# Kernel tuning notes

Measured on AMD Instinct MI355X. Metric: run time of the kernel, lower is better.

Reference implementation:

```python
import jax, jax.numpy as jnp
import numpy as np

V0, V1, V2 = 8000, 4000, 4096   # diag / proc / med vocab sizes
E = 512                          # emb_dim
T, L = 64, 48                    # visits, codes per visit
FAI = 0.05                       # history-selection threshold
EPS = 1e-5                       # LayerNorm eps (torch default)

def _normalize(adj):
    # GCN.normalize: row-normalize (adj + I)
    adj = adj + np.eye(adj.shape[0], dtype=np.float64)
    rowsum = adj.sum(1)
    r_inv = np.where(rowsum > 0, 1.0 / rowsum, 0.0)
    return (r_inv[:, None] * adj).astype(np.float32)

def setup_inputs() -> dict:
    key = jax.random.key(0)
    ks = iter(jax.random.split(key, 48))
    p = lambda *s: jax.random.normal(next(ks), s, jnp.float32) * 0.02
    rng = np.random.default_rng(0)
    def rand_adj():
        a = rng.random((V2, V2)) < 0.01
        a = (a | a.T).astype(np.float64)
        np.fill_diagonal(a, 0.0)
        return a
    ehr = rand_adj(); ddi = rand_adj()
    return dict(
        diag_codes=jax.random.randint(next(ks), (T, L), 0, V0),
        proc_codes=jax.random.randint(next(ks), (T, L), 0, V1),
        emb0=p(V0, E), emb1=p(V1, E), emb2=p(V2, E),
        gru1_Wih=p(3 * E, E), gru1_Whh=p(3 * E, E), gru1_bih=p(3 * E), gru1_bhh=p(3 * E),
        gru2_Wih=p(3 * E, E), gru2_Whh=p(3 * E, E), gru2_bih=p(3 * E), gru2_bhh=p(3 * E),
        query_W=p(E, 2 * E), query_b=p(E),
        poly_h1_W=p(32, 2 * E), poly_h1_b=p(32), poly_gate_W=p(1, 32), poly_gate_b=p(1),
        cls_W=p(V2, 2 * E), cls_b=p(V2),
        ln_gamma=jnp.ones((E,), jnp.float32), ln_beta=jnp.zeros((E,), jnp.float32),
        ehr_W1=p(V2, E), ehr_b1=p(E), ehr_W2=p(E, E), ehr_b2=p(E),
        ddi_W1=p(V2, E), ddi_b1=p(E), ddi_W2=p(E, E), ddi_b2=p(E),
        inter1=p(1),
        ehr_adj_norm=jnp.asarray(_normalize(ehr)),
        ddi_adj_norm=jnp.asarray(_normalize(ddi)),
        ddi_adj=jnp.asarray(ddi.astype(np.float32)),
    )

def _gru_last(x_seq, mask, Wih, Whh, bih, bhh):
    # torch nn.GRU cell, batch=1; masked-out steps carry h unchanged, which
    # equals running the GRU over only the selected subsequence. Only the
    # final hidden state is needed (original uses output[-1]).
    def step(h, inp):
        x, m = inp
        gi = x @ Wih.T + bih          # [3E]
        gh = h @ Whh.T + bhh
        ir, iz, inn = jnp.split(gi, 3)
        hr, hz, hn = jnp.split(gh, 3)
        r = jax.nn.sigmoid(ir + hr)
        z = jax.nn.sigmoid(iz + hz)
        n = jnp.tanh(inn + r * hn)
        h_new = (1.0 - z) * n + z * h
        return jnp.where(m, h_new, h), None
    h0 = jnp.zeros((Wih.shape[1],), x_seq.dtype)
    h_final, _ = jax.lax.scan(step, h0, (x_seq, mask))
    return h_final

def reference(diag_codes, proc_codes, emb0, emb1, emb2,
              gru1_Wih, gru1_Whh, gru1_bih, gru1_bhh,
              gru2_Wih, gru2_Whh, gru2_bih, gru2_bhh,
              query_W, query_b, poly_h1_W, poly_h1_b, poly_gate_W, poly_gate_b,
              cls_W, cls_b, ln_gamma, ln_beta,
              ehr_W1, ehr_b1, ehr_W2, ehr_b2, ddi_W1, ddi_b1, ddi_W2, ddi_b2,
              inter1, ehr_adj_norm, ddi_adj_norm, ddi_adj):
    i1 = emb0[diag_codes].sum(1)            # [T,E] per-visit sum pooling
    i2 = emb1[proc_codes].sum(1)            # [T,E]
    rep = jnp.concatenate([i1, i2], -1)     # [T,2E] patient representation
    # Aggregation gate for history selection
    hidden = jax.nn.relu(rep @ poly_h1_W.T + poly_h1_b)
    gate = jax.nn.sigmoid(hidden @ poly_gate_W.T + poly_gate_b)[:, 0]  # [T]
    s = jnp.abs(gate[-1] - gate[:-1])
    mask = jnp.concatenate([s <= FAI, jnp.ones((1,), bool)])  # last visit always kept
    h1 = _gru_last(i1, mask, gru1_Wih, gru1_Whh, gru1_bih, gru1_bhh)
    h2 = _gru_last(i2, mask, gru2_Wih, gru2_Whh, gru2_bih, gru2_bhh)
    q_in = jnp.concatenate([h1, h2])                      # [2E]
    query = (jax.nn.relu(q_in) @ query_W.T + query_b)[None, :]  # [1,E]
    def gcn(W1, b1, W2, b2, adj):
        h = jax.nn.relu(adj @ W1 + b1)    # x = I so x@W1 = W1 (dropout eval)
        return adj @ (h @ W2) + b2
    safe = gcn(ehr_W1, ehr_b1, ehr_W2, ehr_b2, ehr_adj_norm) \
         - inter1 * gcn(ddi_W1, ddi_b1, ddi_W2, ddi_b2, ddi_adj_norm)
    drug = safe + emb2                                    # [V2,E]
    kw = jax.nn.softmax(query @ drug.T, -1)               # [1,V2]
    med = kw @ drug                                       # [1,E]
    mu = query.mean(-1, keepdims=True)
    var = ((query - mu) ** 2).mean(-1, keepdims=True)
    ln = (query - mu) / jnp.sqrt(var + EPS) * ln_gamma + ln_beta
    final = jnp.concatenate([ln, med], -1)                # [1,2E]
    result = jax.nn.relu(final) @ cls_W.T + cls_b         # [1,V2]
    neg = jax.nn.sigmoid(result)
    batch_neg = 0.0005 * ((neg.T * neg) * ddi_adj).sum()
    return result, batch_neg
```

## Files before the change

### kernel.cpp

```cpp
#include <hip/hip_runtime.h>
#include <cstdint>
#include <cstddef>

typedef unsigned short u16;
typedef unsigned int   u32;

typedef __bf16 bf16x8 __attribute__((ext_vector_type(8)));
typedef float  f32x4  __attribute__((ext_vector_type(4)));

__device__ __forceinline__ float uAsF(u32 u){ union{u32 u; float f;} c; c.u=u; return c.f; }
__device__ __forceinline__ float b2f(u16 v){ return uAsF(((u32)v)<<16); }
__device__ __forceinline__ u16 f2b(float f){
  union{float f; u32 u;} c; c.f=f; u32 x=c.u;
  u32 r = (x + 0x7fffu + ((x>>16)&1u)) >> 16;
  return (u16)r;
}
__device__ __forceinline__ void unpack8(uint4 p, float* f){
  f[0]=uAsF(p.x<<16); f[1]=uAsF(p.x&0xffff0000u);
  f[2]=uAsF(p.y<<16); f[3]=uAsF(p.y&0xffff0000u);
  f[4]=uAsF(p.z<<16); f[5]=uAsF(p.z&0xffff0000u);
  f[6]=uAsF(p.w<<16); f[7]=uAsF(p.w&0xffff0000u);
}
__device__ __forceinline__ float sigm(float x){ return 1.f/(1.f+__expf(-x)); }

// ... 15 lines not shown
}
__device__ __forceinline__ void ld4(const void* p, size_t i, int f32, float* f){
  if (f32){
    float4 a = *(const float4*)((const float*)p + i);
    f[0]=a.x; f[1]=a.y; f[2]=a.z; f[3]=a.w;
  } else {
    uint2 pk = *(const uint2*)((const u16*)p + i);
    f[0]=uAsF(pk.x<<16); f[1]=uAsF(pk.x&0xffff0000u);
    f[2]=uAsF(pk.y<<16); f[3]=uAsF(pk.y&0xffff0000u);
  }
}
__device__ __forceinline__ uint4 ld8p(const void* p, size_t i, int f32){
  if (f32){
    const float4* q = (const float4*)((const float*)p + i);
    float4 a = q[0], b = q[1];
    uint4 r;
    r.x = (u32)f2b(a.x) | ((u32)f2b(a.y)<<16);
    r.y = (u32)f2b(a.z) | ((u32)f2b(a.w)<<16);
    r.z = (u32)f2b(b.x) | ((u32)f2b(b.y)<<16);
    r.w = (u32)f2b(b.z) | ((u32)f2b(b.w)<<16);
    return r;
  }
  return *(const uint4*)((const u16*)p + i);
}

constexpr size_t OFF_I1    = 0;
constexpr size_t OFF_I2    = 0x20000;
constexpr size_t OFF_GI    = 0x40000;
constexpr size_t OFF_GATE  = 0x100000;
constexpr size_t OFF_HBUF  = 0x100800;
constexpr size_t OFF_HFIN  = 0x102800;
constexpr size_t OFF_CTR   = 0x103800;
constexpr size_t OFF_NEGA  = 0x103900;
constexpr size_t OFF_QUERY = 0x104000;
constexpr size_t OFF_SE    = 0x105000;
constexpr size_t OFF_SD    = 0x109000;
constexpr size_t OFF_SEMB  = 0x10D000;
constexpr size_t OFF_KW    = 0x111000;
constexpr size_t OFF_U     = 0x115000;
constexpr size_t OFF_Y     = 0x119000;
constexpr size_t OFF_Z     = 0x11D000;
constexpr size_t OFF_ME    = 0x11D800;
constexpr size_t OFF_MD    = 0x11E000;
constexpr size_t OFF_MEMB  = 0x11E800;
constexpr size_t OFF_FIN   = 0x11F000;
constexpr size_t OFF_NEG   = 0x120000;
constexpr size_t OFF_W1T   = 0x124000;
constexpr size_t OFF_H     = 0x524000;
constexpr size_t NEED_C    = 0x924000;
constexpr size_t OFF_HD    = 0x924000;
constexpr size_t NEED_C2   = 0xD24000;
constexpr size_t OFF_ABD   = 0xD24000;
constexpr size_t NEED_B    = 0x2D24000;
constexpr size_t OFF_ABE   = 0x2D24000;
constexpr size_t NEED_A    = 0x4D24000;

constexpr size_t OFF_UD    = OFF_GI + 0x0000;
constexpr size_t OFF_Y2    = OFF_GI + 0x4000;
constexpr size_t OFF_Z2    = OFF_GI + 0x8000;
constexpr size_t OFF_WVD   = OFF_GI + 0x8800;
constexpr size_t OFF_WVE   = OFF_GI + 0x9000;

__global__ __launch_bounds__(256) void k_cvt(const void* __restrict__ S, u16* __restrict__ D,
                                             const u16* __restrict__ dt)
{
  int f32 = dprobe(dt);
  size_t i8 = ((size_t)blockIdx.x*256 + threadIdx.x) * 8;
  *(uint4*)(D + i8) = ld8p(S, i8, f32);
}

__global__ __launch_bounds__(256) void k_gather(const int* __restrict__ dc, const int* __restrict__ pc,
    const void* __restrict__ emb0, const void* __restrict__ emb1,
    float* __restrict__ i1, float* __restrict__ i2, const u16* __restrict__ dt)
{
  int f32 = dprobe(dt);
  int t = blockIdx.x;
  int which = blockIdx.y;
  const int* codes = which ? pc : dc;
  const void* emb  = which ? emb1 : emb0;
  float* out       = which ? i2 : i1;
  int e = threadIdx.x;
  float s0=0.f, s1=0.f;
  for (int l=0;l<48;l++){
    int c = codes[t*48+l];
    size_t base = (size_t)c*512;
    s0 += ld1(emb, base+e, f32);
    s1 += ld1(emb, base+e+256, f32);
  }
  out[t*512+e] = s0;
  out[t*512+e+256] = s1;
}

__global__ __launch_bounds__(256) void k_gate(const float* __restrict__ i1, const float* __restrict__ i2,
    const void* __restrict__ phW, const void* __restrict__ phb,
    const void* __restrict__ pgW, const void* __restrict__ pgb,
    float* __restrict__ gate, const u16* __restrict__ dt)
{
  int f32 = dprobe(dt);
  int t = blockIdx.x;
  __shared__ float rep[1024];
  __shared__ float hid[32];
  int tid = threadIdx.x;
  for (int q=0;q<4;q++){
    int k = tid + q*256;
    rep[k] = (k<512) ? i1[t*512+k] : i2[t*512+k-512];
  }
  __syncthreads();
  int w = tid>>6, lane = tid&63;
  for (int jj=0;jj<8;jj++){
    int j = w*8 + jj;
    float s = 0.f;
    for (int k=lane;k<1024;k+=64) s += rep[k]*ld1(phW, (size_t)j*1024+k, f32);
    for (int off=32;off;off>>=1) s += __shfl_down(s, off);
    if (lane==0) hid[j] = fmaxf(s + ld1(phb, j, f32), 0.f);
  }
  __syncthreads();
  if (tid==0){
    float s = 0.f;
    for (int j=0;j<32;j++) s += hid[j]*ld1(pgW, j, f32);
    gate[t] = sigm(s + ld1(pgb, 0, f32));
  }
}

__global__ __launch_bounds__(256) void k_gi(const void* __restrict__ Wih0, const void* __restrict__ Wih1,
    const void* __restrict__ bih0, const void* __restrict__ bih1,
    const float* __restrict__ i1, const float* __restrict__ i2,
    float* __restrict__ gi, const u16* __restrict__ dt)
{
  int f32 = dprobe(dt);
  int g  = blockIdx.y;
  int t0 = blockIdx.x*4;
  const void* W   = g ? Wih1 : Wih0;
  const void* bih = g ? bih1 : bih0;
  const float* x = g ? i2 : i1;
  __shared__ float xl[4*512];
  int tid = threadIdx.x;
  for (int q=0;q<8;q++) xl[tid + q*256] = x[t0*512 + tid + q*256];
  __syncthreads();
  int j = blockIdx.z*256 + tid;
  float b = ld1(bih, j, f32);
  float a0=0.f,a1=0.f,a2=0.f,a3=0.f;
  for (int k=0;k<512;k+=8){
    float f[8]; ld8(W, (size_t)j*512 + k, f32, f);
    #pragma unroll
    for (int xx=0;xx<8;xx++){
      float wv = f[xx];
      a0 += wv*xl[k+xx];
      a1 += wv*xl[512+k+xx];
      a2 += wv*xl[1024+k+xx];
      a3 += wv*xl[1536+k+xx];
    }
  }
  float* og = gi + (size_t)g*64*1536;
  og[(size_t)(t0+0)*1536 + j] = a0 + b;
  og[(size_t)(t0+1)*1536 + j] = a1 + b;
  og[(size_t)(t0+2)*1536 + j] = a2 + b;
  og[(size_t)(t0+3)*1536 + j] = a3 + b;
}

__global__ __launch_bounds__(512, 2) void k_gruf(
    const void* __restrict__ Whh0, const void* __restrict__ Whh1,
    const void* __restrict__ bhh0, const void* __restrict__ bhh1,
    const float* __restrict__ gi, const float* __restrict__ gate,
    u32* __restrict__ hbuf, float* __restrict__ hfin, const u16* __restrict__ dt,
    const void* __restrict__ trS, u16* __restrict__ trD,
    const void* __restrict__ cv0S, u16* __restrict__ cv0D, int nc0,
    const void* __restrict__ cv1S, u16* __restrict__ cv1D, int nc1)
{
  int f32 = dprobe(dt);
  const int tid = threadIdx.x;
  int rb = (int)blockIdx.x - 16;
  if (rb >= 0){
    if (rb < 2048){
      __shared__ u16 tile[32][33];
      int bx = rb & 15, by = rb >> 4;
      int lx = tid & 31, ly = tid >> 5;
      int c = bx*32 + lx;
      #pragma unroll
      for (int i=0;i<2;i++){
        int r = by*32 + ly + i*16;
        size_t idx = (size_t)r*512 + c;
        tile[ly+i*16][lx] = f32 ? f2b(((const float*)trS)[idx]) : ((const u16*)trS)[idx];
      }
      __syncthreads();
      int r2 = by*32 + lx;
      #pragma unroll
      for (int i=0;i<2;i++){
        int c2 = bx*32 + ly + i*16;
        trD[(size_t)c2*4096 + r2] = tile[lx][ly+i*16];
      }
      return;
    }
    rb -= 2048;
    if (rb < nc0){
      size_t i8 = ((size_t)rb*512 + tid)*8;
      *(uint4*)(cv0D + i8) = ld8p(cv0S, i8, f32);
      return;
    }
    rb -= nc0;
    if (rb < nc1){
      size_t i8 = ((size_t)rb*512 + tid)*8;
      *(uint4*)(cv1D + i8) = ld8p(cv1S, i8, f32);
      return;
    }
    return;
  }

  const int b = blockIdx.x;
  const int g = b >> 3;
  const int w = b & 7;
  const int e0 = w * 64;
  const void* Whh = g ? Whh1 : Whh0;
  const void* bhh = g ? bhh1 : bhh0;
  const float* gig = gi + (size_t)g*64*1536;

  const int rg = tid & 31;
  const int cg = tid >> 5;

  __shared__ float h_lds[512];
  __shared__ float part[192*17];
  __shared__ float gh_l[192];
  __shared__ float gl[64];
  __shared__ int   mask_l[64];

  u32 wreg[96];
  #pragma unroll
  for (int i=0;i<6;i++){
    int lr = rg*6 + i;
    int grow = (lr >> 6)*512 + e0 + (lr & 63);
    size_t base = (size_t)grow*512 + cg*32;
    if (f32){
      const float2* src = (const float2*)((const float*)Whh + base);
      #pragma unroll
      for (int q=0;q<16;q++){
        float2 v = src[q];
        wreg[i*16+q] = (u32)f2b(v.x) | ((u32)f2b(v.y)<<16);
      }
    } else {
      const uint4* src = (const uint4*)((const u16*)Whh + base);
      #pragma unroll
      for (int q=0;q<4;q++){
        uint4 pk = src[q];
        wreg[i*16+q*4+0]=pk.x; wreg[i*16+q*4+1]=pk.y;
        wreg[i*16+q*4+2]=pk.z; wreg[i*16+q*4+3]=pk.w;
      }
    }
  }
  if (tid < 64) gl[tid] = gate[tid];
  h_lds[tid] = 0.f;
  __syncthreads();
  if (tid < 64)
    mask_l[tid] = (tid==63) ? 1 : (fabsf(gl[63] - gl[tid]) <= 0.05f ? 1 : 0);
  __syncthreads();

  int s = 0;
  for (int t=0;t<64;t++){
    if (!mask_l[t]) continue;
    s++;
    const int p = s & 1;
    float acc6[6] = {0.f,0.f,0.f,0.f,0.f,0.f};
    const float2* h2 = ((const float2*)h_lds) + cg*16;
    #pragma unroll
    for (int q=0;q<16;q++){
      float2 hv = h2[q];
      #pragma unroll
      for (int i=0;i<6;i++){
        u32 wp = wreg[i*16+q];
        acc6[i] += uAsF(wp<<16)*hv.x + uAsF(wp&0xffff0000u)*hv.y;
      }
    }
    #pragma unroll
    for (int i=0;i<6;i++) part[(rg*6+i)*17 + cg] = acc6[i];
    __syncthreads();
    if (tid < 192){
      const float* pp = part + tid*17;
      float ss = 0.f;
      #pragma unroll
      for (int q=0;q<16;q++) ss += pp[q];
      gh_l[tid] = ss;
    }
    __syncthreads();
    if (tid < 64){
      int e = e0 + tid;
      float hr = gh_l[tid]     + ld1(bhh, e, f32);
      float hz = gh_l[64+tid]  + ld1(bhh, 512+e, f32);
// ... 15 lines not shown
      while ((word & 0xffffu) != (u32)s){
        __builtin_amdgcn_s_sleep(1);
        word = __hip_atomic_load(src, __ATOMIC_RELAXED, __HIP_MEMORY_SCOPE_AGENT);
      }
      h_lds[tid] = uAsF(word & 0xffff0000u);
    }
    __syncthreads();
  }
  if (tid < 64) hfin[g*512 + e0 + tid] = h_lds[e0 + tid];
}

__global__ __launch_bounds__(256) void k_transpose(const void* __restrict__ S, u16* __restrict__ D,
                                                   int R, int C, const u16* __restrict__ dt)
{
  int f32 = dprobe(dt);
  __shared__ u16 tile[32][33];
  int lx = threadIdx.x & 31, ly = threadIdx.x >> 5;
  int c = blockIdx.x*32 + lx;
  #pragma unroll
  for (int i=0;i<4;i++){
    int r = blockIdx.y*32 + ly + i*8;
    size_t idx = (size_t)r*C + c;
    tile[ly+i*8][lx] = f32 ? f2b(((const float*)S)[idx]) : ((const u16*)S)[idx];
  }
  __syncthreads();
  int r2 = blockIdx.y*32 + lx;
  #pragma unroll
  for (int i=0;i<4;i++){
    int c2 = blockIdx.x*32 + ly + i*8;
    D[(size_t)c2*R + r2] = tile[lx][ly+i*8];
  }
}

__global__ __launch_bounds__(256)
void k_gemm(const void* __restrict__ A, const u16* __restrict__ Bt,
            const void* __restrict__ bias, u16* __restrict__ C, int K,
            const u16* __restrict__ adt, const u16* __restrict__ bdt)
{
  int af32 = dprobe(adt), bf32 = dprobe(bdt);
  const int m0 = blockIdx.x * 64;
  const int n0 = blockIdx.y * 128;
  const int tid = threadIdx.x;
  const int lane = tid & 63;
  const int wv = tid >> 6;
  const int wr = wv >> 1, wc = wv & 1;
  const int l15 = lane & 15, lq = lane >> 4;

  __shared__ u16 As[2][64*64];
  __shared__ u16 Bs[2][128*64];

  f32x4 acc[2][4];
  #pragma unroll
  for (int i=0;i<2;i++)
    #pragma unroll
    for (int j=0;j<4;j++)
      acc[i][j] = (f32x4){0.f,0.f,0.f,0.f};

  const int srow = tid >> 3;
  const int sc8  = tid & 7;
  const size_t grow_a = (size_t)(m0 + srow) * K + sc8*8;
  const size_t grow_b = (size_t)(n0 + srow) * K + sc8*8;
  const int adst0 = srow*64 + ((sc8 ^ (srow&7))*8);
  const int adst1 = (32+srow)*64 + ((sc8 ^ ((32+srow)&7))*8);
  int bdst[4];
  #pragma unroll
  for (int q=0;q<4;q++){
    int row = q*32 + srow;
    bdst[q] = row*64 + ((sc8 ^ (row&7))*8);
  }

  {
    uint4 va0 = ld8p(A, grow_a, af32);
    uint4 va1 = ld8p(A, grow_a + (size_t)32*K, af32);
    uint4 vb[4];
    #pragma unroll
    for (int q=0;q<4;q++) vb[q] = *(const uint4*)(Bt + grow_b + (size_t)q*32*K);
    *(uint4*)(As[0] + adst0) = va0;
    *(uint4*)(As[0] + adst1) = va1;
    #pragma unroll
    for (int q=0;q<4;q++) *(uint4*)(Bs[0] + bdst[q]) = vb[q];
  }
  __syncthreads();

  for (int k0 = 0; k0 < K; k0 += 64){
    const int cur = (k0 >> 6) & 1;
    const int nxt = 1 - cur;
    uint4 va0, va1, vb[4];
    const bool more = (k0 + 64) < K;
    if (more){
      va0 = ld8p(A, grow_a + k0 + 64, af32);
      va1 = ld8p(A, grow_a + (size_t)32*K + k0 + 64, af32);
      #pragma unroll
      for (int q=0;q<4;q++) vb[q] = *(const uint4*)(Bt + grow_b + (size_t)q*32*K + k0 + 64);
    }
    #pragma unroll
    for (int ks=0; ks<2; ++ks){
      bf16x8 af[2], bfr[4];
      #pragma unroll
      for (int i=0;i<2;i++){
        int ar = wr*32 + i*16 + l15;
        af[i]  = *(const bf16x8*)(As[cur] + ar*64 + (((ks*4+lq) ^ (ar&7))*8));
      }
      #pragma unroll
      for (int j=0;j<4;j++){
        int br = wc*64 + j*16 + l15;
        bfr[j] = *(const bf16x8*)(Bs[cur] + br*64 + (((ks*4+lq) ^ (br&7))*8));
      }
      #pragma unroll
      for (int i=0;i<2;i++)
        #pragma unroll
        for (int j=0;j<4;j++)
          acc[i][j] = __builtin_amdgcn_mfma_f32_16x16x32_bf16(af[i], bfr[j], acc[i][j], 0,0,0);
    }
    if (more){
      *(uint4*)(As[nxt] + adst0) = va0;
      *(uint4*)(As[nxt] + adst1) = va1;
      #pragma unroll
      for (int q=0;q<4;q++) *(uint4*)(Bs[nxt] + bdst[q]) = vb[q];
      __syncthreads();
    }
  }

  #pragma unroll
  for (int i=0;i<2;i++){
    int row = wr*32 + i*16 + lq*4;
    #pragma unroll
    for (int j=0;j<4;j++){
      int col = wc*64 + j*16 + l15;
      int n = n0 + col;
      float bv = ld1(bias, n, bf32);
      #pragma unroll
      for (int r=0;r<4;r++){
        float v = fmaxf(acc[i][j][r] + bv, 0.f);
        C[(size_t)(m0+row+r)*512 + n] = f2b(v);
      }
    }
  }
}

__global__ __launch_bounds__(256) void k_matvec(const void* __restrict__ A, const float* __restrict__ x,
    float* __restrict__ y, int M, int Kc, const u16* __restrict__ dt)
{
  int f32 = dprobe(dt);
  __shared__ float xl[4096];
  int tid = threadIdx.x;
  for (int k=tid; k<Kc; k+=256) xl[k] = x[k];
  __syncthreads();
  int w = tid>>6, lane = tid&63;
  int r0 = blockIdx.x*16 + w*4;
  for (int i=0;i<4;i++){
    int r = r0 + i;
    float s = 0.f;
    for (int k0 = lane*8; k0 < Kc; k0 += 512){
      float f[8]; ld8(A, (size_t)r*Kc + k0, f32, f);
      #pragma unroll
      for (int xx=0;xx<8;xx++) s += f[xx]*xl[k0+xx];
    }
    for (int off=32;off;off>>=1) s += __shfl_down(s, off);
    if (lane==0) y[r] = s;
  }
}

__global__ __launch_bounds__(256) void k_mvp(
    const void* __restrict__ A0, const float* __restrict__ x0, float* __restrict__ y0, const u16* d0,
    const void* __restrict__ A1, const float* __restrict__ x1, float* __restrict__ y1, const u16* d1,
    int Kc, int half)
{
  __shared__ float xl[4096];
  int bx = blockIdx.x, tid = threadIdx.x;
  const void* A; const float* x; float* y; const u16* dtp; int xb;
  if (bx < half){ A=A0; x=x0; y=y0; dtp=d0; xb=bx; }
  else          { A=A1; x=x1; y=y1; dtp=d1; xb=bx-half; }
  int f32 = dprobe(dtp);
  for (int k=tid; k<Kc; k+=256) xl[k] = x[k];
  __syncthreads();
  int w = tid>>6, lane = tid&63;
  int r0 = xb*16 + w*4;
  for (int i=0;i<4;i++){
    int r = r0 + i;
    float s = 0.f;
    for (int k0 = lane*8; k0 < Kc; k0 += 512){
      float f[8]; ld8(A, (size_t)r*Kc + k0, f32, f);
      #pragma unroll
      for (int xx=0;xx<8;xx++) s += f[xx]*xl[k0+xx];
    }
    for (int off=32;off;off>>=1) s += __shfl_down(s, off);
    if (lane==0) y[r] = s;
  }
}

__global__ __launch_bounds__(256) void k_colreduce(const void* __restrict__ A, const float* __restrict__ w,
    float* __restrict__ y, int C, const u16* __restrict__ dt)
{
  int f32 = dprobe(dt);
  __shared__ float wl[256];
  int tid = threadIdx.x;
  int v0 = blockIdx.y*256;
  wl[tid] = w[v0+tid];
  __syncthreads();
  int k = blockIdx.x*256 + tid;
  float acc = 0.f;
  size_t base = (size_t)v0*C + k;
  for (int i=0;i<256;i++) acc += wl[i]*ld1(A, base + (size_t)i*C, f32);
  atomicAdd(&y[k], acc);
}

__global__ __launch_bounds__(256) void k_cr3(
    const void* __restrict__ Ae, const u16* aedt, float* __restrict__ ye,
    const void* __restrict__ Ad, const u16* addt, float* __restrict__ yd,
    const void* __restrict__ E2, const u16* edt, float* __restrict__ ym,
    const float* __restrict__ kw)
{
  __shared__ float wl[256];
  int tid = threadIdx.x, bx = blockIdx.x;
  int v0 = blockIdx.y*256;
  wl[tid] = kw[v0+tid];
  __syncthreads();
  const void* A; float* y; int C, k, f32;
  if (bx < 16){ A=Ae; y=ye; C=4096; k=bx*256+tid; f32=dprobe(aedt); }
  else if (bx < 32){ A=Ad; y=yd; C=4096; k=(bx-16)*256+tid; f32=dprobe(addt); }
  else { A=E2; y=ym; C=512; k=(bx-32)*256+tid; f32=dprobe(edt); }
  float acc = 0.f;
  size_t base = (size_t)v0*C + k;
  for (int i=0;i<256;i++) acc += wl[i]*ld1(A, base + (size_t)i*C, f32);
  atomicAdd(&y[k], acc);
}

__global__ __launch_bounds__(256) void k_crp(
    const void* __restrict__ A0, const float* __restrict__ w0, float* __restrict__ y0, const u16* d0,
    const void* __restrict__ A1, const float* __restrict__ w1, float* __restrict__ y1, const u16* d1,
    int C, int half)
{
  __shared__ float wl[256];
  int tid = threadIdx.x, bx = blockIdx.x;
  int v0 = blockIdx.y*256;
  const void* A; const float* w; float* y; const u16* dtp; int xk;
  if (bx < half){ A=A0; w=w0; y=y0; dtp=d0; xk=bx; }
  else          { A=A1; w=w1; y=y1; dtp=d1; xk=bx-half; }
  int f32 = dprobe(dtp);
  wl[tid] = w[v0+tid];
  __syncthreads();
  int k = xk*256 + tid;
  float acc = 0.f;
  size_t base = (size_t)v0*C + k;
  for (int i=0;i<256;i++) acc += wl[i]*ld1(A, base + (size_t)i*C, f32);
  atomicAdd(&y[k], acc);
}

__global__ void k_zero(float* __restrict__ p, int n){
  int i = blockIdx.x*1024 + threadIdx.x;
  if (i < n) p[i] = 0.f;
}

__global__ __launch_bounds__(256) void k_mv3(
    const void* __restrict__ E2, const void* __restrict__ W2d, const void* __restrict__ W2e,
    const float* __restrict__ query,
    float* __restrict__ s_emb, float* __restrict__ wv_d, float* __restrict__ wv_e,
    float* __restrict__ zA, float* __restrict__ zB, float* __restrict__ nega,
    u32* __restrict__ ctr, const u16* __restrict__ dt)
{
  int bx = blockIdx.x, tid = threadIdx.x;
  if (bx >= 320){
    int rb = bx - 320;
    if (rb < 4){
      #pragma unroll
      for (int q=0;q<6;q++){ int i = rb*1536 + q*256 + tid; if (i < 6144) zA[i] = 0.f; }
    } else if (rb < 7){
      int c = rb - 4;
      #pragma unroll
      for (int q=0;q<6;q++){ int i = c*1536 + q*256 + tid; if (i < 4608) zB[i] = 0.f; }
    } else if (tid == 0){
      *nega = 0.f; ctr[0] = 0u; ctr[1] = 0u;
    }
    return;
  }
  int f32 = dprobe(dt);
  __shared__ float xl[512];
  for (int k=tid; k<512; k+=256) xl[k] = query[k];
  __syncthreads();
// ... 168 lines not shown
  const void* emb1 = d_in[3];
  const void* emb2 = d_in[4];
  const void* g1Wih=d_in[5];  const void* g1Whh=d_in[6];
  const void* g1bih=d_in[7];  const void* g1bhh=d_in[8];
  const void* g2Wih=d_in[9];  const void* g2Whh=d_in[10];
  const void* g2bih=d_in[11]; const void* g2bhh=d_in[12];
  const void* qW =d_in[13];   const void* qb =d_in[14];
  const void* phW=d_in[15];   const void* phb=d_in[16];
  const void* pgW=d_in[17];   const void* pgb=d_in[18];
  const void* clsW=d_in[19];  const void* clsb=d_in[20];
  const void* lng=d_in[21];   const void* lnb=d_in[22];
  const void* eW1=d_in[23];   const void* eb1=d_in[24];
  const void* eW2=d_in[25];   const void* eb2=d_in[26];
  const void* dW1=d_in[27];   const void* db1=d_in[28];
  const void* dW2=d_in[29];   const void* db2=d_in[30];
  const void* inter1=d_in[31];
  const void* eAdj=d_in[32];
  const void* dAdjN=d_in[33];
  const void* dAdj=d_in[34];

  const u16* dt = (const u16*)lng;

  if (ws_size < NEED_C){
    unsigned mb = (unsigned)(ws_size >> 20);
    int b = 0;
    while ((2u << b) <= mb + 1 && b < 15) b++;
    k_diag<<<17, 256, 0, stream>>>((u16*)d_out, 30000.f + 1000.f*(float)b);
    return;
  }

  const bool hasHd  = ws_size >= NEED_C2;
  const bool hasAb  = ws_size >= NEED_B;
  const bool hasAb2 = ws_size >= NEED_A;
  const bool mergedTail = hasHd && (hasAb2 || !hasAb);

  char* ws = (char*)d_ws;
  float* i1    = (float*)(ws + OFF_I1);
  float* i2    = (float*)(ws + OFF_I2);
  float* gi    = (float*)(ws + OFF_GI);
  float* gate  = (float*)(ws + OFF_GATE);
  u32*   hbuf  = (u32*)  (ws + OFF_HBUF);
  float* hfin  = (float*)(ws + OFF_HFIN);
  u32*   ctr   = (u32*)  (ws + OFF_CTR);
  float* nega  = (float*)(ws + OFF_NEGA);
  float* query = (float*)(ws + OFF_QUERY);
  float* s_e   = (float*)(ws + OFF_SE);
  float* s_d   = (float*)(ws + OFF_SD);
  float* s_emb = (float*)(ws + OFF_SEMB);
  float* kw    = (float*)(ws + OFF_KW);
  float* u_e   = (float*)(ws + OFF_U);
  float* y     = (float*)(ws + OFF_Y);
  float* z     = (float*)(ws + OFF_Z);
  float* me    = (float*)(ws + OFF_ME);
  float* md    = (float*)(ws + OFF_MD);
  float* memb  = (float*)(ws + OFF_MEMB);
  float* fin   = (float*)(ws + OFF_FIN);
  float* neg   = (float*)(ws + OFF_NEG);
  u16*   W1T   = (u16*)  (ws + OFF_W1T);
  u16*   h     = (u16*)  (ws + OFF_H);
  u16*   h_d   = hasHd ? (u16*)(ws + OFF_HD) : h;
  u16*   AbD   = (u16*)  (ws + OFF_ABD);
  u16*   AbE   = hasAb2 ? (u16*)(ws + OFF_ABE) : AbD;
  float* u_d   = (float*)(ws + OFF_UD);
  float* y2    = (float*)(ws + OFF_Y2);
  float* z2    = (float*)(ws + OFF_Z2);
  float* wv_d  = (float*)(ws + OFF_WVD);
  float* wv_e  = (float*)(ws + OFF_WVE);
  void*  outv  = d_out;

  const void* Ad   = hasAb ? (const void*)AbD : dAdjN;
  const u16*  adt  = hasAb ? (const u16*)nullptr : dt;
  const void* Ae   = hasAb ? (const void*)AbE : eAdj;
  const u16*  aedt = hasAb ? (const u16*)nullptr : dt;

  k_gather<<<dim3(64,2), 256, 0, stream>>>(diag, proc, emb0, emb1, i1, i2, dt);
  k_gate<<<64, 256, 0, stream>>>(i1, i2, phW, phb, pgW, pgb, gate, dt);
  k_gi<<<dim3(16,2,6), 256, 0, stream>>>(g1Wih, g2Wih, g1bih, g2bih, i1, i2, gi, dt);

  {
    int nc0 = hasAb  ? 4096 : 0;
    int nc1 = hasAb2 ? 4096 : 0;
    k_gruf<<<16 + 2048 + nc0 + nc1, 512, 0, stream>>>(
        g1Whh, g2Whh, g1bhh, g2bhh, gi, gate, hbuf, hfin, dt,
        dW1, W1T,
        dAdjN, AbD, nc0,
        eAdj,  AbE, nc1);
  }
  k_query<<<8, 256, 0, stream>>>(hfin, qW, qb, query, dt);
  k_mv3<<<328, 256, 0, stream>>>(emb2, dW2, eW2, query, s_emb, wv_d, wv_e,
                                 y, y2, nega, ctr, dt);

  if (mergedTail){
    k_gemm<<<dim3(64,4), 256, 0, stream>>>(Ad, W1T, db1, h_d, 4096, adt, dt);
    k_transpose<<<dim3(16,128), 256, 0, stream>>>(eW1, W1T, 4096, 512, dt);
    k_gemm<<<dim3(64,4), 256, 0, stream>>>(Ae, W1T, eb1, h, 4096, aedt, dt);
    k_mvp<<<512, 256, 0, stream>>>(h, wv_e, u_e, nullptr, h_d, wv_d, u_d, nullptr, 512, 256);
    k_mvp<<<512, 256, 0, stream>>>(Ae, u_e, s_e, aedt, Ad, u_d, s_d, adt, 4096, 256);
    k_softmax<<<1, 1024, 0, stream>>>(s_e, s_d, s_emb, inter1, kw, dt);
    k_cr3<<<dim3(34,16), 256, 0, stream>>>(Ae, aedt, y, Ad, adt, y2, emb2, dt, memb, kw);
    k_crp<<<dim3(4,16), 256, 0, stream>>>(h, y, z, nullptr, h_d, y2, z2, nullptr, 512, 2);
    k_crp<<<dim3(4,2), 256, 0, stream>>>(eW2, z, me, dt, dW2, z2, md, dt, 512, 2);
  } else {
    k_gemm<<<dim3(64,4), 256, 0, stream>>>(Ad, W1T, db1, h_d, 4096, adt, dt);
    k_matvec<<<256, 256, 0, stream>>>(h_d, wv_d, u_e, 4096, 512, nullptr);
    k_matvec<<<256, 256, 0, stream>>>(Ad, u_e, s_d, 4096, 4096, adt);

    if (hasAb) k_cvt<<<8192, 256, 0, stream>>>(eAdj, AbE, dt);
    k_transpose<<<dim3(16,128), 256, 0, stream>>>(eW1, W1T, 4096, 512, dt);
    k_gemm<<<dim3(64,4), 256, 0, stream>>>(Ae, W1T, eb1, h, 4096, aedt, dt);
    k_matvec<<<256, 256, 0, stream>>>(h, wv_e, u_e, 4096, 512, nullptr);
    k_matvec<<<256, 256, 0, stream>>>(Ae, u_e, s_e, 4096, 4096, aedt);

    k_softmax<<<1, 1024, 0, stream>>>(s_e, s_d, s_emb, inter1, kw, dt);

    k_colreduce<<<dim3(16,16), 256, 0, stream>>>(Ae, kw, y, 4096, aedt);
    k_colreduce<<<dim3(2,16),  256, 0, stream>>>(h,  y,  z, 512,  nullptr);
    k_colreduce<<<dim3(2,2),   256, 0, stream>>>(eW2, z, me, 512, dt);
    k_colreduce<<<dim3(2,16),  256, 0, stream>>>(emb2, kw, memb, 512, dt);

    k_zero<<<5, 1024, 0, stream>>>(y, 4608);
    if (hasAb && !hasAb2) k_cvt<<<8192, 256, 0, stream>>>(dAdjN, AbD, dt);
    if (!hasHd){
      k_transpose<<<dim3(16,128), 256, 0, stream>>>(dW1, W1T, 4096, 512, dt);
      k_gemm<<<dim3(64,4), 256, 0, stream>>>(Ad, W1T, db1, h, 4096, adt, dt);
    }
    k_colreduce<<<dim3(16,16), 256, 0, stream>>>(Ad, kw, y, 4096, adt);
    k_colreduce<<<dim3(2,16),  256, 0, stream>>>(h_d, y, z, 512, nullptr);
    k_colreduce<<<dim3(2,2),   256, 0, stream>>>(dW2, z, md, 512, dt);
  }

  k_ln<<<1, 512, 0, stream>>>(query, me, md, memb, eb2, db2, inter1, lng, lnb, fin, dt);
  k_cls<<<64, 256, 0, stream>>>(fin, clsW, clsb, outv, neg, dt);
  k_negsum<<<128, 256, 0, stream>>>(dAdj, neg, nega, ctr, outv, dt);
}
```

Measured before the change: 1.067 ms.

## Fuse launch pipeline: merge gather/gate, fold input-gate GEMM into GRU kernel, merge GEMMs

Merges the gather and gate kernels, and moves the GRU input-projection GEMM into the persistent GRU launch as extra blocks. The GRU blocks now wait on an atomic counter for those blocks, so the separate gi launch is gone. The two GCN GEMMs, the matvecs and buffer zeroing are combined into one large launch using a second transposed W1 buffer. Softmax is fused into the matvec kernel and LayerNorm into the column reduce, each run by the last-block-done pattern. This cuts launch count and serialization, at the cost of extra workspace and spin-wait barriers that rely on the producer blocks being scheduled.

```diff
diff --git a/kernel.cpp b/kernel.cpp
--- a/kernel.cpp
+++ b/kernel.cpp
@@ -71,6 +71,7 @@
 constexpr size_t OFF_HFIN  = 0x102800;
 constexpr size_t OFF_CTR   = 0x103800;
 constexpr size_t OFF_NEGA  = 0x103900;
+constexpr size_t OFF_BAR   = 0x103A00;
 constexpr size_t OFF_QUERY = 0x104000;
 constexpr size_t OFF_SE    = 0x105000;
 constexpr size_t OFF_SD    = 0x109000;
@@ -93,6 +94,8 @@
 constexpr size_t NEED_B    = 0x2D24000;
 constexpr size_t OFF_ABE   = 0x2D24000;
 constexpr size_t NEED_A    = 0x4D24000;
+constexpr size_t OFF_W1TE  = 0x4D24000;
+constexpr size_t NEED_A2   = 0x5124000;
 
 constexpr size_t OFF_UD    = OFF_GI + 0x0000;
 constexpr size_t OFF_Y2    = OFF_GI + 0x4000;
@@ -108,42 +111,38 @@
   *(uint4*)(D + i8) = ld8p(S, i8, f32);
 }
 
-__global__ __launch_bounds__(256) void k_gather(const int* __restrict__ dc, const int* __restrict__ pc,
+__global__ __launch_bounds__(256) void k_gg(const int* __restrict__ dc, const int* __restrict__ pc,
     const void* __restrict__ emb0, const void* __restrict__ emb1,
-    float* __restrict__ i1, float* __restrict__ i2, const u16* __restrict__ dt)
-{
-  int f32 = dprobe(dt);
-  int t = blockIdx.x;
-  int which = blockIdx.y;
-  const int* codes = which ? pc : dc;
-  const void* emb  = which ? emb1 : emb0;
-  float* out       = which ? i2 : i1;
-  int e = threadIdx.x;
-  float s0=0.f, s1=0.f;
-  for (int l=0;l<48;l++){
-    int c = codes[t*48+l];
-    size_t base = (size_t)c*512;
-    s0 += ld1(emb, base+e, f32);
-    s1 += ld1(emb, base+e+256, f32);
-  }
-  out[t*512+e] = s0;
-  out[t*512+e+256] = s1;
-}
-
-__global__ __launch_bounds__(256) void k_gate(const float* __restrict__ i1, const float* __restrict__ i2,
     const void* __restrict__ phW, const void* __restrict__ phb,
     const void* __restrict__ pgW, const void* __restrict__ pgb,
-    float* __restrict__ gate, const u16* __restrict__ dt)
-{
+    float* __restrict__ i1, float* __restrict__ i2, float* __restrict__ gate,
+    u32* __restrict__ bars, float* __restrict__ nega, u32* __restrict__ ctr,
+    const u16* __restrict__ dt)
+{
+  int tid = threadIdx.x;
+  if (blockIdx.x == 64){
+    if (tid < 32) bars[tid] = 0u;
+    if (tid == 32) *nega = 0.f;
+    if (tid == 33){ ctr[0] = 0u; ctr[1] = 0u; }
+    return;
+  }
   int f32 = dprobe(dt);
   int t = blockIdx.x;
   __shared__ float rep[1024];
   __shared__ float hid[32];
-  int tid = threadIdx.x;
-  for (int q=0;q<4;q++){
-    int k = tid + q*256;
-    rep[k] = (k<512) ? i1[t*512+k] : i2[t*512+k-512];
-  }
+  float s0=0.f, s1=0.f, s2=0.f, s3=0.f;
+  for (int l=0;l<48;l++){
+    int c0 = dc[t*48+l];
+    int c1 = pc[t*48+l];
+    size_t b0 = (size_t)c0*512, b1 = (size_t)c1*512;
+    s0 += ld1(emb0, b0+tid, f32);
+    s1 += ld1(emb0, b0+tid+256, f32);
+    s2 += ld1(emb1, b1+tid, f32);
+    s3 += ld1(emb1, b1+tid+256, f32);
+  }
+  i1[t*512+tid] = s0; i1[t*512+tid+256] = s1;
+  i2[t*512+tid] = s2; i2[t*512+tid+256] = s3;
+  rep[tid] = s0; rep[tid+256] = s1; rep[512+tid] = s2; rep[768+tid] = s3;
   __syncthreads();
   int w = tid>>6, lane = tid&63;
   for (int jj=0;jj<8;jj++){
@@ -161,48 +160,17 @@
   }
 }
 
-__global__ __launch_bounds__(256) void k_gi(const void* __restrict__ Wih0, const void* __restrict__ Wih1,
+__global__ __launch_bounds__(512, 2) void k_gruf2(
+    const void* __restrict__ Whh0, const void* __restrict__ Whh1,
+    const void* __restrict__ bhh0, const void* __restrict__ bhh1,
+    const void* __restrict__ Wih0, const void* __restrict__ Wih1,
     const void* __restrict__ bih0, const void* __restrict__ bih1,
     const float* __restrict__ i1, const float* __restrict__ i2,
-    float* __restrict__ gi, const u16* __restrict__ dt)
-{
-  int f32 = dprobe(dt);
-  int g  = blockIdx.y;
-  int t0 = blockIdx.x*4;
-  const void* W   = g ? Wih1 : Wih0;
-  const void* bih = g ? bih1 : bih0;
-  const float* x = g ? i2 : i1;
-  __shared__ float xl[4*512];
-  int tid = threadIdx.x;
-  for (int q=0;q<8;q++) xl[tid + q*256] = x[t0*512 + tid + q*256];
-  __syncthreads();
-  int j = blockIdx.z*256 + tid;
-  float b = ld1(bih, j, f32);
-  float a0=0.f,a1=0.f,a2=0.f,a3=0.f;
-  for (int k=0;k<512;k+=8){
-    float f[8]; ld8(W, (size_t)j*512 + k, f32, f);
-    #pragma unroll
-    for (int xx=0;xx<8;xx++){
-      float wv = f[xx];
-      a0 += wv*xl[k+xx];
-      a1 += wv*xl[512+k+xx];
-      a2 += wv*xl[1024+k+xx];
-      a3 += wv*xl[1536+k+xx];
-    }
-  }
-  float* og = gi + (size_t)g*64*1536;
-  og[(size_t)(t0+0)*1536 + j] = a0 + b;
-  og[(size_t)(t0+1)*1536 + j] = a1 + b;
-  og[(size_t)(t0+2)*1536 + j] = a2 + b;
-  og[(size_t)(t0+3)*1536 + j] = a3 + b;
-}
-
-__global__ __launch_bounds__(512, 2) void k_gruf(
-    const void* __restrict__ Whh0, const void* __restrict__ Whh1,
-    const void* __restrict__ bhh0, const void* __restrict__ bhh1,
-    const float* __restrict__ gi, const float* __restrict__ gate,
-    u32* __restrict__ hbuf, float* __restrict__ hfin, const u16* __restrict__ dt,
+    float* __restrict__ gi, const float* __restrict__ gate,
+    u32* __restrict__ hbuf, float* __restrict__ hfin,
+    u32* __restrict__ bars, const u16* __restrict__ dt,
     const void* __restrict__ trS, u16* __restrict__ trD,
+    const void* __restrict__ trS2, u16* __restrict__ trD2, int nt2,
     const void* __restrict__ cv0S, u16* __restrict__ cv0D, int nc0,
     const void* __restrict__ cv1S, u16* __restrict__ cv1D, int nc1)
 {
@@ -210,27 +178,65 @@
   const int tid = threadIdx.x;
   int rb = (int)blockIdx.x - 16;
   if (rb >= 0){
-    if (rb < 2048){
+    if (rb < 96){
+      __shared__ float xg[2048];
+      int g = (rb>>4)&1, z = rb>>5, t0 = (rb&15)*4;
+      const float* x   = g ? i2 : i1;
+      const void* W    = g ? Wih1 : Wih0;
+      const void* bih  = g ? bih1 : bih0;
+      for (int q=0;q<4;q++) xg[tid + q*512] = x[t0*512 + tid + q*512];
+      __syncthreads();
+      int j = z*512 + tid;
+      float b = ld1(bih, j, f32);
+      float a0=0.f,a1=0.f,a2=0.f,a3=0.f;
+      for (int k=0;k<512;k+=8){
+        float f[8]; ld8(W, (size_t)j*512 + k, f32, f);
+        #pragma unroll
+        for (int xx=0;xx<8;xx++){
+          float wv = f[xx];
+          a0 += wv*xg[k+xx];
+          a1 += wv*xg[512+k+xx];
+          a2 += wv*xg[1024+k+xx];
+          a3 += wv*xg[1536+k+xx];
+        }
+      }
+      float* og = gi + (size_t)g*64*1536;
+      og[(size_t)(t0+0)*1536 + j] = a0 + b;
+      og[(size_t)(t0+1)*1536 + j] = a1 + b;
+      og[(size_t)(t0+2)*1536 + j] = a2 + b;
+      og[(size_t)(t0+3)*1536 + j] = a3 + b;
+      __syncthreads();
+      if (tid == 0){
+        __threadfence();
+        __hip_atomic_fetch_add(&bars[31], 1u, __ATOMIC_RELAXED, __HIP_MEMORY_SCOPE_AGENT);
+      }
+      return;
+    }
+    rb -= 96;
+    if (rb < 2048 + nt2){
+      const void* S = (rb < 2048) ? trS : trS2;
+      u16* D = (rb < 2048) ? trD : trD2;
+      int t = (rb < 2048) ? rb : rb - 2048;
       __shared__ u16 tile[32][33];
-      int bx = rb & 15, by = rb >> 4;
+      int bx = t & 15, by = t >> 4;
       int lx = tid & 31, ly = tid >> 5;
       int c = bx*32 + lx;
       #pragma unroll
       for (int i=0;i<2;i++){
         int r = by*32 + ly + i*16;
         size_t idx = (size_t)r*512 + c;
-        tile[ly+i*16][lx] = f32 ? f2b(((const float*)trS)[idx]) : ((const u16*)trS)[idx];
+        tile[ly+i*16][lx] = f32 ? f2b(((const float*)S)[idx]) : ((const u16*)S)[idx];
       }
       __syncthreads();
       int r2 = by*32 + lx;
       #pragma unroll
       for (int i=0;i<2;i++){
         int c2 = bx*32 + ly + i*16;
-        trD[(size_t)c2*4096 + r2] = tile[lx][ly+i*16];
+        D[(size_t)c2*4096 + r2] = tile[lx][ly+i*16];
       }
       return;
     }
-    rb -= 2048;
+    rb -= 2048 + nt2;
     if (rb < nc0){
       size_t i8 = ((size_t)rb*512 + tid)*8;
       *(uint4*)(cv0D + i8) = ld8p(cv0S, i8, f32);
@@ -290,6 +296,12 @@
   __syncthreads();
   if (tid < 64)
     mask_l[tid] = (tid==63) ? 1 : (fabsf(gl[63] - gl[tid]) <= 0.05f ? 1 : 0);
+  __syncthreads();
+  if (tid == 0){
+    while (__hip_atomic_load(&bars[31], __ATOMIC_RELAXED, __HIP_MEMORY_SCOPE_AGENT) < 96u)
+      __builtin_amdgcn_s_sleep(2);
+    __threadfence();
+  }
   __syncthreads();
 
   int s = 0;
@@ -371,22 +383,16 @@
   }
 }
 
-__global__ __launch_bounds__(256)
-void k_gemm(const void* __restrict__ A, const u16* __restrict__ Bt,
-            const void* __restrict__ bias, u16* __restrict__ C, int K,
-            const u16* __restrict__ adt, const u16* __restrict__ bdt)
-{
-  int af32 = dprobe(adt), bf32 = dprobe(bdt);
-  const int m0 = blockIdx.x * 64;
-  const int n0 = blockIdx.y * 128;
-  const int tid = threadIdx.x;
+__device__ __forceinline__ void gemm_body(const void* A, const u16* Bt,
+    const void* bias, u16* C, int af32, int bf32, int task, u16* As, u16* Bs, int tid)
+{
+  const int K = 4096;
+  const int m0 = (task & 63) * 64;
+  const int n0 = (task >> 6) * 128;
   const int lane = tid & 63;
   const int wv = tid >> 6;
   const int wr = wv >> 1, wc = wv & 1;
   const int l15 = lane & 15, lq = lane >> 4;
-
-  __shared__ u16 As[2][64*64];
-  __shared__ u16 Bs[2][128*64];
 
   f32x4 acc[2][4];
   #pragma unroll
@@ -414,10 +420,10 @@
     uint4 vb[4];
     #pragma unroll
     for (int q=0;q<4;q++) vb[q] = *(const uint4*)(Bt + grow_b + (size_t)q*32*K);
-    *(uint4*)(As[0] + adst0) = va0;
-    *(uint4*)(As[0] + adst1) = va1;
+    *(uint4*)(As + adst0) = va0;
+    *(uint4*)(As + adst1) = va1;
     #pragma unroll
-    for (int q=0;q<4;q++) *(uint4*)(Bs[0] + bdst[q]) = vb[q];
+    for (int q=0;q<4;q++) *(uint4*)(Bs + bdst[q]) = vb[q];
   }
   __syncthreads();
 
@@ -432,18 +438,20 @@
       #pragma unroll
       for (int q=0;q<4;q++) vb[q] = *(const uint4*)(Bt + grow_b + (size_t)q*32*K + k0 + 64);
     }
+    u16* Asc = As + cur*4096;
+    u16* Bsc = Bs + cur*8192;
     #pragma unroll
     for (int ks=0; ks<2; ++ks){
       bf16x8 af[2], bfr[4];
       #pragma unroll
       for (int i=0;i<2;i++){
         int ar = wr*32 + i*16 + l15;
-        af[i]  = *(const bf16x8*)(As[cur] + ar*64 + (((ks*4+lq) ^ (ar&7))*8));
+        af[i]  = *(const bf16x8*)(Asc + ar*64 + (((ks*4+lq) ^ (ar&7))*8));
       }
       #pragma unroll
       for (int j=0;j<4;j++){
         int br = wc*64 + j*16 + l15;
-        bfr[j] = *(const bf16x8*)(Bs[cur] + br*64 + (((ks*4+lq) ^ (br&7))*8));
+        bfr[j] = *(const bf16x8*)(Bsc + br*64 + (((ks*4+lq) ^ (br&7))*8));
       }
       #pragma unroll
       for (int i=0;i<2;i++)
@@ -452,10 +460,12 @@
           acc[i][j] = __builtin_amdgcn_mfma_f32_16x16x32_bf16(af[i], bfr[j], acc[i][j], 0,0,0);
     }
     if (more){
-      *(uint4*)(As[nxt] + adst0) = va0;
-      *(uint4*)(As[nxt] + adst1) = va1;
-      #pragma unroll
-      for (int q=0;q<4;q++) *(uint4*)(Bs[nxt] + bdst[q]) = vb[q];
+      u16* Asn = As + nxt*4096;
+      u16* Bsn = Bs + nxt*8192;
+      *(uint4*)(Asn + adst0) = va0;
+      *(uint4*)(Asn + adst1) = va1;
+      #pragma unroll
+      for (int q=0;q<4;q++) *(uint4*)(Bsn + bdst[q]) = vb[q];
       __syncthreads();
     }
   }
@@ -477,6 +487,72 @@
   }
 }
 
+__global__ __launch_bounds__(256)
+void k_gemm(const void* __restrict__ A, const u16* __restrict__ Bt,
+            const void* __restrict__ bias, u16* __restrict__ C, int K,
+            const u16* __restrict__ adt, const u16* __restrict__ bdt)
+{
+  (void)K;
+  __shared__ __attribute__((aligned(16))) char smem[49152];
+  int t = (int)blockIdx.x | ((int)blockIdx.y << 6);
+  gemm_body(A, Bt, bias, C, dprobe(adt), dprobe(bdt), t, (u16*)smem, (u16*)(smem+16384), threadIdx.x);
+}
+
+__global__ __launch_bounds__(256) void k_big(
+    const void* __restrict__ Ad, const u16* adt, const u16* __restrict__ W1Td,
+    const void* __restrict__ db1, u16* __restrict__ h_d,
+    const void* __restrict__ Ae, const u16* aedt, const u16* __restrict__ W1Te,
+    const void* __restrict__ eb1, u16* __restrict__ h_,
+    const void* __restrict__ E2, const void* __restrict__ W2d, const void* __restrict__ W2e,
+    const float* __restrict__ query,
+    float* __restrict__ s_emb, float* __restrict__ wv_d, float* __restrict__ wv_e,
+    float* __restrict__ zA, float* __restrict__ zB,
+    const u16* __restrict__ dt)
+{
+  __shared__ __attribute__((aligned(16))) char smem[49152];
+  const int bid = blockIdx.x, tid = threadIdx.x;
+  if (bid < 512){
+    if (bid < 256)
+      gemm_body(Ad, W1Td, db1, h_d, dprobe(adt), dprobe(dt), bid, (u16*)smem, (u16*)(smem+16384), tid);
+    else
+      gemm_body(Ae, W1Te, eb1, h_, dprobe(aedt), dprobe(dt), bid-256, (u16*)smem, (u16*)(smem+16384), tid);
+    return;
+  }
+  int t = bid - 512;
+  int f32 = dprobe(dt);
+  if (t >= 320){
+    if (t < 324){
+      int rb = t - 320;
+      #pragma unroll
+      for (int q=0;q<6;q++){ int i = rb*1536 + q*256 + tid; if (i < 6144) zA[i] = 0.f; }
+    } else {
+      int c = t - 324;
+      #pragma unroll
+      for (int q=0;q<6;q++){ int i = c*1536 + q*256 + tid; if (i < 4608) zB[i] = 0.f; }
+    }
+    return;
+  }
+  float* xl = (float*)smem;
+  for (int k=tid; k<512; k+=256) xl[k] = query[k];
+  __syncthreads();
+  const void* A; float* y; int xb;
+  if (t < 256){ A=E2; y=s_emb; xb=t; }
+  else if (t < 288){ A=W2d; y=wv_d; xb=t-256; }
+  else { A=W2e; y=wv_e; xb=t-288; }
+  int w = tid>>6, lane = tid&63;
+  int r0 = xb*16 + w*4;
+  for (int i=0;i<4;i++){
+    int r = r0 + i;
+    float s = 0.f;
+    int k0 = lane*8;
+    float f[8]; ld8(A, (size_t)r*512 + k0, f32, f);
+    #pragma unroll
+    for (int xx=0;xx<8;xx++) s += f[xx]*xl[k0+xx];
+    for (int off=32;off;off>>=1) s += __shfl_down(s, off);
+    if (lane==0) y[r] = s;
+  }
+}
+
 __global__ __launch_bounds__(256) void k_matvec(const void* __restrict__ A, const float* __restrict__ x,
     float* __restrict__ y, int M, int Kc, const u16* __restrict__ dt)
 {
@@ -525,6 +601,67 @@
     }
     for (int off=32;off;off>>=1) s += __shfl_down(s, off);
     if (lane==0) y[r] = s;
+  }
+}
+
+__global__ __launch_bounds__(256) void k_mvps(
+    const void* __restrict__ Ae, const float* __restrict__ ue, float* __restrict__ se, const u16* aedt,
+    const void* __restrict__ Ad, const float* __restrict__ ud, float* __restrict__ sd, const u16* adt,
+    const float* __restrict__ semb, const void* __restrict__ inter1, float* __restrict__ kw,
+    u32* __restrict__ tick, const u16* __restrict__ dt)
+{
+  __shared__ float xl[4096];
+  __shared__ int lastf;
+  int bx = blockIdx.x, tid = threadIdx.x;
+  const void* A; const float* x; float* yy; int f32;
+  if (bx < 256){ A=Ae; x=ue; yy=se; f32=dprobe(aedt); }
+  else         { A=Ad; x=ud; yy=sd; f32=dprobe(adt); }
+  int xb = bx & 255;
+  for (int k=tid; k<4096; k+=256) xl[k] = x[k];
+  __syncthreads();
+  int w = tid>>6, lane = tid&63;
+  int r0 = xb*16 + w*4;
+  for (int i=0;i<4;i++){
+    int r = r0 + i;
+    float s = 0.f;
+    for (int k0 = lane*8; k0 < 4096; k0 += 512){
+      float f[8]; ld8(A, (size_t)r*4096 + k0, f32, f);
+      #pragma unroll
+      for (int xx=0;xx<8;xx++) s += f[xx]*xl[k0+xx];
+    }
+    for (int off=32;off;off>>=1) s += __shfl_down(s, off);
+    if (lane==0) yy[r] = s;
+  }
+  __syncthreads();
+  if (tid == 0){
+    __threadfence();
+    u32 old = atomicAdd(tick, 1u);
+    lastf = (old == 511u);
+    if (lastf) __threadfence();
+  }
+  __syncthreads();
+  if (lastf){
+    int df = dprobe(dt);
+    float* red = xl;
+    float it1 = ld1(inter1, 0, df);
+    float v[16]; float m = -1e30f;
+    #pragma unroll
+    for (int q=0;q<16;q++){
+      int i = tid + q*256;
+      v[q] = se[i] - it1*sd[i] + semb[i];
+      m = fmaxf(m, v[q]);
+    }
+    red[tid] = m; __syncthreads();
+    for (int s=128;s;s>>=1){ if (tid<s) red[tid] = fmaxf(red[tid], red[tid+s]); __syncthreads(); }
+    m = red[0]; __syncthreads();
+    float sum = 0.f;
+    #pragma unroll
+    for (int q=0;q<16;q++){ v[q] = __expf(v[q]-m); sum += v[q]; }
+    red[tid] = sum; __syncthreads();
+    for (int s=128;s;s>>=1){ if (tid<s) red[tid] += red[tid+s]; __syncthreads(); }
+    float inv = 1.f/red[0];
+    #pragma unroll
+    for (int q=0;q<16;q++) kw[tid + q*256] = v[q]*inv;
   }
 }
 
@@ -584,6 +721,65 @@
   size_t base = (size_t)v0*C + k;
   for (int i=0;i<256;i++) acc += wl[i]*ld1(A, base + (size_t)i*C, f32);
   atomicAdd(&y[k], acc);
+}
+
+__global__ __launch_bounds__(256) void k_crpln(
+    const void* __restrict__ eW2, const float* __restrict__ z, float* __restrict__ me,
+    const void* __restrict__ dW2, const float* __restrict__ z2, float* __restrict__ mdp,
+    const float* __restrict__ query, const float* __restrict__ memb,
+    const void* __restrict__ eb2, const void* __restrict__ db2, const void* __restrict__ inter1,
+    const void* __restrict__ gam, const void* __restrict__ bet,
+    float* __restrict__ fin, u32* __restrict__ tick, const u16* __restrict__ dt)
+{
+  __shared__ float wl[256];
+  __shared__ int lastf;
+  int tid = threadIdx.x, bx = blockIdx.x;
+  int f32 = dprobe(dt);
+  {
+    int side = bx >> 2;
+    int sub  = bx & 3;
+    int xk = sub & 1;
+    int v0 = (sub >> 1) * 256;
+    const void* A = side ? dW2 : eW2;
+    const float* w = side ? z2 : z;
+    float* y = side ? mdp : me;
+    wl[tid] = w[v0+tid];
+    __syncthreads();
+    int k = xk*256 + tid;
+    float acc = 0.f;
+    size_t base = (size_t)v0*512 + k;
+    for (int i=0;i<256;i++) acc += wl[i]*ld1(A, base + (size_t)i*512, f32);
+    atomicAdd(&y[k], acc);
+  }
+  __syncthreads();
+  if (tid == 0){
+    __threadfence();
+    u32 old = atomicAdd(tick, 1u);
+    lastf = (old == 7u);
+    if (lastf) __threadfence();
+  }
+  __syncthreads();
+  if (lastf){
+    float* red = wl;
+    float q0 = query[tid], q1 = query[tid+256];
+    red[tid] = q0 + q1; __syncthreads();
+    for (int s=128;s;s>>=1){ if (tid<s) red[tid] += red[tid+s]; __syncthreads(); }
+    float mu = red[0]/512.f; __syncthreads();
+    float d0 = q0 - mu, d1 = q1 - mu;
+    red[tid] = d0*d0 + d1*d1; __syncthreads();
+    for (int s=128;s;s>>=1){ if (tid<s) red[tid] += red[tid+s]; __syncthreads(); }
+    float rstd = rsqrtf(red[0]/512.f + 1e-5f);
+    float it1 = ld1(inter1, 0, f32);
+    int e0 = tid, e1 = tid + 256;
+    float ln0 = d0*rstd*ld1(gam,e0,f32) + ld1(bet,e0,f32);
+    float ln1 = d1*rstd*ld1(gam,e1,f32) + ld1(bet,e1,f32);
+    float mv0 = (me[e0] + ld1(eb2,e0,f32)) - it1*(mdp[e0] + ld1(db2,e0,f32)) + memb[e0];
+    float mv1 = (me[e1] + ld1(eb2,e1,f32)) - it1*(mdp[e1] + ld1(db2,e1,f32)) + memb[e1];
+    fin[e0] = fmaxf(ln0, 0.f);
+    fin[e1] = fmaxf(ln1, 0.f);
+    fin[512+e0] = fmaxf(mv0, 0.f);
+    fin[512+e1] = fmaxf(mv1, 0.f);
+  }
 }
 
 __global__ void k_zero(float* __restrict__ p, int n){
@@ -818,6 +1014,7 @@
   const bool hasHd  = ws_size >= NEED_C2;
   const bool hasAb  = ws_size >= NEED_B;
   const bool hasAb2 = ws_size >= NEED_A;
+  const bool hasW2  = ws_size >= NEED_A2;
   const bool mergedTail = hasHd && (hasAb2 || !hasAb);
 
   char* ws = (char*)d_ws;
@@ -829,6 +1026,7 @@
   float* hfin  = (float*)(ws + OFF_HFIN);
   u32*   ctr   = (u32*)  (ws + OFF_CTR);
   float* nega  = (float*)(ws + OFF_NEGA);
+  u32*   bars  = (u32*)  (ws + OFF_BAR);
   float* query = (float*)(ws + OFF_QUERY);
   float* s_e   = (float*)(ws + OFF_SE);
   float* s_d   = (float*)(ws + OFF_SD);
@@ -843,6 +1041,7 @@
   float* fin   = (float*)(ws + OFF_FIN);
   float* neg   = (float*)(ws + OFF_NEG);
   u16*   W1T   = (u16*)  (ws + OFF_W1T);
+  u16*   W1TE  = (u16*)  (ws + OFF_W1TE);
   u16*   h     = (u16*)  (ws + OFF_H);
   u16*   h_d   = hasHd ? (u16*)(ws + OFF_HD) : h;
   u16*   AbD   = (u16*)  (ws + OFF_ABD);
@@ -859,34 +1058,51 @@
   const void* Ae   = hasAb ? (const void*)AbE : eAdj;
   const u16*  aedt = hasAb ? (const u16*)nullptr : dt;
 
-  k_gather<<<dim3(64,2), 256, 0, stream>>>(diag, proc, emb0, emb1, i1, i2, dt);
-  k_gate<<<64, 256, 0, stream>>>(i1, i2, phW, phb, pgW, pgb, gate, dt);
-  k_gi<<<dim3(16,2,6), 256, 0, stream>>>(g1Wih, g2Wih, g1bih, g2bih, i1, i2, gi, dt);
+  k_gg<<<65, 256, 0, stream>>>(diag, proc, emb0, emb1, phW, phb, pgW, pgb,
+                               i1, i2, gate, bars, nega, ctr, dt);
 
   {
+    int nt2 = hasW2 ? 2048 : 0;
     int nc0 = hasAb  ? 4096 : 0;
     int nc1 = hasAb2 ? 4096 : 0;
-    k_gruf<<<16 + 2048 + nc0 + nc1, 512, 0, stream>>>(
-        g1Whh, g2Whh, g1bhh, g2bhh, gi, gate, hbuf, hfin, dt,
+    k_gruf2<<<16 + 96 + 2048 + nt2 + nc0 + nc1, 512, 0, stream>>>(
+        g1Whh, g2Whh, g1bhh, g2bhh,
+        g1Wih, g2Wih, g1bih, g2bih,
+        i1, i2, gi, gate, hbuf, hfin, bars, dt,
         dW1, W1T,
+        eW1, W1TE, nt2,
         dAdjN, AbD, nc0,
         eAdj,  AbE, nc1);
   }
-  k_query<<<8, 256, 0, stream>>>(hfin, qW, qb, query, dt);
-  k_mv3<<<328, 256, 0, stream>>>(emb2, dW2, eW2, query, s_emb, wv_d, wv_e,
-                                 y, y2, nega, ctr, dt);
 
   if (mergedTail){
-    k_gemm<<<dim3(64,4), 256, 0, stream>>>(Ad, W1T, db1, h_d, 4096, adt, dt);
-    k_transpose<<<dim3(16,128), 256, 0, stream>>>(eW1, W1T, 4096, 512, dt);
-    k_gemm<<<dim3(64,4), 256, 0, stream>>>(Ae, W1T, eb1, h, 4096, aedt, dt);
+    k_query<<<8, 256, 0, stream>>>(hfin, qW, qb, query, dt);
+    if (hasW2){
+      k_big<<<839, 256, 0, stream>>>(Ad, adt, W1T, db1, h_d,
+                                     Ae, aedt, W1TE, eb1, h,
+                                     emb2, dW2, eW2, query,
+                                     s_emb, wv_d, wv_e, y, y2, dt);
+    } else {
+      k_mv3<<<328, 256, 0, stream>>>(emb2, dW2, eW2, query, s_emb, wv_d, wv_e,
+                                     y, y2, nega, ctr, dt);
+      k_gemm<<<dim3(64,4), 256, 0, stream>>>(Ad, W1T, db1, h_d, 4096, adt, dt);
+      k_transpose<<<dim3(16,128), 256, 0, stream>>>(eW1, W1T, 4096, 512, dt);
+      k_gemm<<<dim3(64,4), 256, 0, stream>>>(Ae, W1T, eb1, h, 4096, aedt, dt);
+    }
     k_mvp<<<512, 256, 0, stream>>>(h, wv_e, u_e, nullptr, h_d, wv_d, u_d, nullptr, 512, 256);
-    k_mvp<<<512, 256, 0, stream>>>(Ae, u_e, s_e, aedt, Ad, u_d, s_d, adt, 4096, 256);
-    k_softmax<<<1, 1024, 0, stream>>>(s_e, s_d, s_emb, inter1, kw, dt);
+    k_mvps<<<512, 256, 0, stream>>>(Ae, u_e, s_e, aedt, Ad, u_d, s_d, adt,
+                                    s_emb, inter1, kw, &bars[29], dt);
     k_cr3<<<dim3(34,16), 256, 0, stream>>>(Ae, aedt, y, Ad, adt, y2, emb2, dt, memb, kw);
     k_crp<<<dim3(4,16), 256, 0, stream>>>(h, y, z, nullptr, h_d, y2, z2, nullptr, 512, 2);
-    k_crp<<<dim3(4,2), 256, 0, stream>>>(eW2, z, me, dt, dW2, z2, md, dt, 512, 2);
+    k_crpln<<<8, 256, 0, stream>>>(eW2, z, me, dW2, z2, md,
+                                   query, memb, eb2, db2, inter1, lng, lnb,
+                                   fin, &bars[28], dt);
+    k_cls<<<64, 256, 0, stream>>>(fin, clsW, clsb, outv, neg, dt);
+    k_negsum<<<128, 256, 0, stream>>>(dAdj, neg, nega, ctr, outv, dt);
   } else {
+    k_query<<<8, 256, 0, stream>>>(hfin, qW, qb, query, dt);
+    k_mv3<<<328, 256, 0, stream>>>(emb2, dW2, eW2, query, s_emb, wv_d, wv_e,
+                                   y, y2, nega, ctr, dt);
     k_gemm<<<dim3(64,4), 256, 0, stream>>>(Ad, W1T, db1, h_d, 4096, adt, dt);
     k_matvec<<<256, 256, 0, stream>>>(h_d, wv_d, u_e, 4096, 512, nullptr);
     k_matvec<<<256, 256, 0, stream>>>(Ad, u_e, s_d, 4096, 4096, adt);
@@ -913,9 +1129,9 @@
     k_colreduce<<<dim3(16,16), 256, 0, stream>>>(Ad, kw, y, 4096, adt);
     k_colreduce<<<dim3(2,16),  256, 0, stream>>>(h_d, y, z, 512, nullptr);
     k_colreduce<<<dim3(2,2),   256, 0, stream>>>(dW2, z, md, 512, dt);
-  }
-
-  k_ln<<<1, 512, 0, stream>>>(query, me, md, memb, eb2, db2, inter1, lng, lnb, fin, dt);
-  k_cls<<<64, 256, 0, stream>>>(fin, clsW, clsb, outv, neg, dt);
-  k_negsum<<<128, 256, 0, stream>>>(dAdj, neg, nega, ctr, outv, dt);
-}
+
+    k_ln<<<1, 512, 0, stream>>>(query, me, md, memb, eb2, db2, inter1, lng, lnb, fin, dt);
+    k_cls<<<64, 256, 0, stream>>>(fin, clsW, clsb, outv, neg, dt);
+    k_negsum<<<128, 256, 0, stream>>>(dAdj, neg, nega, ctr, outv, dt);
+  }
+}
```

New measurement: 1.029 ms. -3.5%, faster.
